# Kernel tuning notes

Measured on AMD Instinct MI355X. Metric: run time of the kernel, lower is better.

## Reference

```python
import jax, jax.numpy as jnp
import numpy as np

B, S, D, H = 2, 2048, 1024, 16
DK = D // H

def setup_inputs() -> dict:
    key = jax.random.key(0)
    ks = jax.random.split(key, 5)
    std = 1.0 / np.sqrt(D)
    return {
        "x": jax.random.normal(ks[0], (B, S, D), dtype=jnp.float32),
        "wq": jax.random.normal(ks[1], (D, D), dtype=jnp.float32) * std,
        "wk": jax.random.normal(ks[2], (D, D), dtype=jnp.float32) * std,
        "wv": jax.random.normal(ks[3], (D, D), dtype=jnp.float32) * std,
        "wo": jax.random.normal(ks[4], (D, D), dtype=jnp.float32) * std,
    }

def reference(x, wq, wk, wv, wo):
    b, s, d = x.shape
    # torch Linear(bias=False): x @ W.T
    q = (x @ wq.T).reshape(b, s, H, DK).transpose(0, 2, 1, 3)  # [b,h,s,dk]
    k = (x @ wk.T).reshape(b, s, H, DK).transpose(0, 2, 1, 3)
    v = (x @ wv.T).reshape(b, s, H, DK).transpose(0, 2, 1, 3)
    scale = jnp.sqrt(jnp.asarray(DK, dtype=x.dtype))
    scores = jnp.einsum('bhqd,bhkd->bhqk', q, k) / scale  # [b,h,s,s]
    # causal mask (masking=True): lower-triangular kept, rest -inf
    causal = jnp.tril(jnp.ones((s, s), dtype=bool))
    scores = jnp.where(causal[None, None], scores, -jnp.inf)
    attn = jax.nn.softmax(scores, axis=-1)
    out = jnp.einsum('bhqk,bhkd->bhqd', attn, v)  # [b,h,s,dk]
    out = out.transpose(0, 2, 1, 3).reshape(b, s, d)
    return out @ wo.T
```

## Files before the change

### kernel.cpp

```cpp
#include <hip/hip_runtime.h>

#define LB __launch_bounds__(256)

typedef __bf16 bf16x8 __attribute__((ext_vector_type(8)));
typedef float f32x4 __attribute__((ext_vector_type(4)));
typedef float f32x16 __attribute__((ext_vector_type(16)));
typedef unsigned int u32;

constexpr int B = 2, S = 2048, D = 1024, H = 16, DK = 64;
constexpr int M = B * S;
constexpr int K = D;

__device__ __forceinline__ unsigned short f2bf(float f) {
    union { float f; unsigned u; } v; v.f = f;
    unsigned r = v.u + 0x7fffu + ((v.u >> 16) & 1u);
    return (unsigned short)(r >> 16);
}

__device__ __forceinline__ u32 pk2bf(float lo, float hi) {
    union { __bf16 h[2]; u32 w; } u;
    u.h[0] = (__bf16)lo; u.h[1] = (__bf16)hi;
    return u.w;
}

__device__ __forceinline__ void gld_lds16(const unsigned short* g, unsigned short* l) {
    __builtin_amdgcn_global_load_lds(
        (const __attribute__((address_space(1))) unsigned int*)g,
        (__attribute__((address_space(3))) unsigned int*)l, 16, 0, 0);
}

__global__ LB void cvt_all(const float* __restrict__ x,  const float* __restrict__ wq,
                           const float* __restrict__ wk, const float* __restrict__ wv,
                           const float* __restrict__ wo, unsigned short* __restrict__ dst) {
    const size_t NX = (size_t)M * D;
    const size_t NW = (size_t)D * D;
    size_t i = ((size_t)blockIdx.x * 256 + threadIdx.x) * 4;
    if (i >= NX + 4 * NW) return;
    const float* src; size_t off;
    if      (i < NX)          { src = x;  off = i; }
    else if (i < NX + NW)     { src = wq; off = i - NX; }
    else if (i < NX + 2 * NW) { src = wk; off = i - NX - NW; }
    else if (i < NX + 3 * NW) { src = wv; off = i - NX - 2 * NW; }
    else                      { src = wo; off = i - NX - 3 * NW; }
    float4 f = *reinterpret_cast<const float4*>(src + off);
    ushort4 o;
    o.x = f2bf(f.x); o.y = f2bf(f.y); o.z = f2bf(f.z); o.w = f2bf(f.w);
    *reinterpret_cast<ushort4*>(dst + i) = o;
}

__global__ LB void gemm_qkv(const unsigned short* __restrict__ A,
                            const unsigned short* __restrict__ wqb,
                            const unsigned short* __restrict__ wkb,
                            const unsigned short* __restrict__ wvb,
                            unsigned short* __restrict__ qo,
                            unsigned short* __restrict__ ko,
                            unsigned short* __restrict__ vo) {
    __shared__ __align__(16) unsigned short lA[128 * 32];
    __shared__ __align__(16) unsigned short lB[128 * 32];
    const int z = blockIdx.y;
    const unsigned short* W = (z == 0) ? wqb : ((z == 1) ? wkb : wvb);
    int m0 = (blockIdx.x >> 3) * 128;
    int n0 = (blockIdx.x & 7) * 128;
    int t = threadIdx.x;
    int w = t >> 6, lane = t & 63;
    int r = lane & 15, g = lane >> 4;
    int wr = w >> 1, wc = w & 1;
    int rowT = t >> 2, colOff = (t & 3) * 8;

    f32x4 acc[4][4];
#pragma unroll
    for (int mi = 0; mi < 4; ++mi)
#pragma unroll
        for (int ni = 0; ni < 4; ++ni) acc[mi][ni] = f32x4{0.f, 0.f, 0.f, 0.f};

    for (int k0 = 0; k0 < K; k0 += 32) {
        gld_lds16(A + (size_t)(m0 + rowT) * K + k0 + colOff,      lA + (w * 64) * 8);
        gld_lds16(A + (size_t)(m0 + 64 + rowT) * K + k0 + colOff, lA + (256 + w * 64) * 8);
        gld_lds16(W + (size_t)(n0 + rowT) * K + k0 + colOff,      lB + (w * 64) * 8);
        gld_lds16(W + (size_t)(n0 + 64 + rowT) * K + k0 + colOff, lB + (256 + w * 64) * 8);
        __syncthreads();
        bf16x8 af[4], bfr[4];
#pragma unroll
        for (int mi = 0; mi < 4; ++mi)
            af[mi] = *reinterpret_cast<const bf16x8*>(&lA[(wr * 64 + mi * 16 + r) * 32 + g * 8]);
#pragma unroll
        for (int ni = 0; ni < 4; ++ni)
            bfr[ni] = *reinterpret_cast<const bf16x8*>(&lB[(wc * 64 + ni * 16 + r) * 32 + g * 8]);
#pragma unroll
        for (int mi = 0; mi < 4; ++mi)
#pragma unroll
            for (int ni = 0; ni < 4; ++ni)
                acc[mi][ni] = __builtin_amdgcn_mfma_f32_16x16x32_bf16(af[mi], bfr[ni], acc[mi][ni], 0, 0, 0);
        __syncthreads();
    }

    const float QSCALE = 0.125f * 1.44269504088896341f;
    float scale = (z == 0) ? QSCALE : 1.0f;
    unsigned short* dst = (z == 0) ? qo : ((z == 1) ? ko : vo);
#pragma unroll
    for (int mi = 0; mi < 4; ++mi)
#pragma unroll
        for (int ni = 0; ni < 4; ++ni)
#pragma unroll
            for (int j = 0; j < 4; ++j) {
                int row = m0 + wr * 64 + mi * 16 + g * 4 + j;
                int col = n0 + wc * 64 + ni * 16 + r;
                int b = row >> 11, s = row & (S - 1);
                int h = col >> 6, dk = col & 63;
                size_t bh = (size_t)(b * H + h);
                unsigned short val = f2bf(acc[mi][ni][j] * scale);
                if (z == 0) {
                    dst[(bh * S + s) * DK + dk] = val;
                } else if (z == 1) {
                    int kt32 = s >> 5, q5k = s & 31;
                    int dsi = dk >> 4, hlk = (dk >> 3) & 1, e = dk & 7;
                    dst[(((bh * 64 + kt32) * 4 + dsi) * 64 + (hlk * 32 + q5k)) * 8 + e] = val;
                } else {
                    int ktile = s >> 6, ks2 = (s >> 4) & 3, hlv = (s >> 3) & 1, e = s & 7;
                    int rh = dk >> 5, q5r = dk & 31;
                    dst[(((bh * 32 + ktile) * 8 + rh * 4 + ks2) * 64 + (hlv * 32 + q5r)) * 8 + e] = val;
                }
            }
}

__global__ LB void out_gemm(const unsigned short* __restrict__ A,
                            const unsigned short* __restrict__ W,
                            float* __restrict__ out) {
    __shared__ __align__(16) unsigned short lA[128 * 32];
    __shared__ __align__(16) unsigned short lB[128 * 32];
    int m0 = (blockIdx.x >> 3) * 128;
    int n0 = (blockIdx.x & 7) * 128;
    int t = threadIdx.x;
    int w = t >> 6, lane = t & 63;
    int r = lane & 15, g = lane >> 4;
    int wr = w >> 1, wc = w & 1;
    int rowT = t >> 2, colOff = (t & 3) * 8;

    f32x4 acc[4][4];
#pragma unroll
    for (int mi = 0; mi < 4; ++mi)
#pragma unroll
        for (int ni = 0; ni < 4; ++ni) acc[mi][ni] = f32x4{0.f, 0.f, 0.f, 0.f};

    for (int k0 = 0; k0 < K; k0 += 32) {
        gld_lds16(A + (size_t)(m0 + rowT) * K + k0 + colOff,      lA + (w * 64) * 8);
        gld_lds16(A + (size_t)(m0 + 64 + rowT) * K + k0 + colOff, lA + (256 + w * 64) * 8);
        gld_lds16(W + (size_t)(n0 + rowT) * K + k0 + colOff,      lB + (w * 64) * 8);
        gld_lds16(W + (size_t)(n0 + 64 + rowT) * K + k0 + colOff, lB + (256 + w * 64) * 8);
        __syncthreads();
        bf16x8 af[4], bfr[4];
#pragma unroll
        for (int mi = 0; mi < 4; ++mi)
            af[mi] = *reinterpret_cast<const bf16x8*>(&lA[(wr * 64 + mi * 16 + r) * 32 + g * 8]);
#pragma unroll
        for (int ni = 0; ni < 4; ++ni)
            bfr[ni] = *reinterpret_cast<const bf16x8*>(&lB[(wc * 64 + ni * 16 + r) * 32 + g * 8]);
#pragma unroll
        for (int mi = 0; mi < 4; ++mi)
#pragma unroll
            for (int ni = 0; ni < 4; ++ni)
                acc[mi][ni] = __builtin_amdgcn_mfma_f32_16x16x32_bf16(af[mi], bfr[ni], acc[mi][ni], 0, 0, 0);
        __syncthreads();
    }

#pragma unroll
    for (int mi = 0; mi < 4; ++mi)
#pragma unroll
        for (int ni = 0; ni < 4; ++ni)
#pragma unroll
            for (int j = 0; j < 4; ++j) {
                int row = m0 + wr * 64 + mi * 16 + g * 4 + j;
                int col = n0 + wc * 64 + ni * 16 + r;
                out[(size_t)row * D + col] = acc[mi][ni][j];
            }
}

__global__ __launch_bounds__(64) void flash_attn(
        const unsigned short* __restrict__ q,
        const unsigned short* __restrict__ kmat,
        const unsigned short* __restrict__ vt,
        unsigned short* __restrict__ ao) {
    int bid = blockIdx.x;
    int kk = bid >> 8, cc = bid & 255;
    int r9 = (kk << 8) | ((kk & 1) ? (255 - cc) : cc);
    int qt = 63 - (r9 >> 5);
    int bh = r9 & 31;
    int b = bh >> 4, hd = bh & 15;
    int q0 = qt << 5;
    int nt = (qt + 2) >> 1;

    int l = threadIdx.x;
    int q5 = l & 31, hl = l >> 5;
    int qglob = q0 + q5;

    const unsigned short* qp = q    + (size_t)bh * S * DK;
    const unsigned short* kf = kmat + (size_t)bh * S * DK;
    const unsigned short* vf = vt   + (size_t)bh * S * DK;

    bf16x8 ones;
#pragma unroll
    for (int i = 0; i < 8; ++i) ones[i] = (__bf16)1.0f;

    const f32x16 z16 = {0,0,0,0,0,0,0,0,0,0,0,0,0,0,0,0};

    bf16x8 qf[4];
#pragma unroll
    for (int dsi = 0; dsi < 4; ++dsi)
        qf[dsi] = *reinterpret_cast<const bf16x8*>(qp + (size_t)qglob * DK + dsi * 16 + hl * 8);

    f32x16 acc0 = z16, acc1 = z16, accl = z16;

    auto loadK = [&](bf16x8 (&kr)[8], int kb) {
        const unsigned short* base = kf + (size_t)(kb >> 5) * 4 * 512 + l * 8;
#pragma unroll
        for (int dsi = 0; dsi < 4; ++dsi) {
            kr[dsi]     = *reinterpret_cast<const bf16x8*>(base + dsi * 512);
            kr[4 + dsi] = *reinterpret_cast<const bf16x8*>(base + (4 + dsi) * 512);
        }
    };
    auto loadV = [&](bf16x8 (&vr)[8], int kb) {
        const unsigned short* base = vf + (size_t)(kb >> 6) * 8 * 512 + l * 8;
#pragma unroll
        for (int i2 = 0; i2 < 8; ++i2)
            vr[i2] = *reinterpret_cast<const bf16x8*>(base + i2 * 512);
    };
    auto compute = [&](bf16x8 (&kr)[8], bf16x8 (&vr)[8], int kb) {
        f32x16 st0 = z16, st1 = z16;
#pragma unroll
        for (int dsi = 0; dsi < 4; ++dsi) {
            st0 = __builtin_amdgcn_mfma_f32_32x32x16_bf16(kr[dsi],     qf[dsi], st0, 0, 0, 0);
            st1 = __builtin_amdgcn_mfma_f32_32x32x16_bf16(kr[4 + dsi], qf[dsi], st1, 0, 0, 0);
        }
        if (kb + 31 > q0) {
#pragma unroll
            for (int r = 0; r < 16; ++r) {
                int kv = kb + (r & 3) + 8 * (r >> 2) + 4 * hl;
                st0[r] = (kv <= qglob) ? st0[r] : -1e30f;
            }
        }
        if (kb + 63 > q0) {
#pragma unroll
            for (int r = 0; r < 16; ++r) {
                int kv = kb + 32 + (r & 3) + 8 * (r >> 2) + 4 * hl;
                st1[r] = (kv <= qglob) ? st1[r] : -1e30f;
            }
        }
#pragma unroll
        for (int r = 0; r < 16; ++r) { st0[r] = exp2f(st0[r]); st1[r] = exp2f(st1[r]); }
        u32 pk[2][8];
#pragma unroll
        for (int rg = 0; rg < 4; ++rg) {
            pk[0][2*rg]   = pk2bf(st0[4*rg],   st0[4*rg+1]);
            pk[0][2*rg+1] = pk2bf(st0[4*rg+2], st0[4*rg+3]);
            pk[1][2*rg]   = pk2bf(st1[4*rg],   st1[4*rg+1]);
            pk[1][2*rg+1] = pk2bf(st1[4*rg+2], st1[4*rg+3]);
        }
        union PF { bf16x8 vv; u32 w[4]; } pf[4];
#pragma unroll
        for (int ti2 = 0; ti2 < 2; ++ti2)
#pragma unroll
            for (int s = 0; s < 2; ++s) {
                u32 s0 = hl ? pk[ti2][4*s]   : pk[ti2][4*s+2];
                u32 s1 = hl ? pk[ti2][4*s+1] : pk[ti2][4*s+3];
                u32 r0 = (u32)__shfl_xor((int)s0, 32);
                u32 r1 = (u32)__shfl_xor((int)s1, 32);
                PF f;
                f.w[0] = hl ? r0 : pk[ti2][4*s];
                f.w[1] = hl ? r1 : pk[ti2][4*s+1];
                f.w[2] = hl ? pk[ti2][4*s+2] : r0;
                f.w[3] = hl ? pk[ti2][4*s+3] : r1;
                pf[ti2*2+s] = f;
            }
#pragma unroll
        for (int ks = 0; ks < 4; ++ks) {
            acc0 = __builtin_amdgcn_mfma_f32_32x32x16_bf16(vr[ks],     pf[ks].vv, acc0, 0, 0, 0);
            acc1 = __builtin_amdgcn_mfma_f32_32x32x16_bf16(vr[4 + ks], pf[ks].vv, acc1, 0, 0, 0);
            accl = __builtin_amdgcn_mfma_f32_32x32x16_bf16(ones,       pf[ks].vv, accl, 0, 0, 0);
        }
    };

    bf16x8 ka[8], kb2[8], va[8], vb2[8];
    loadK(ka, 0);
    loadV(va, 0);
    int it = 0;
    while (true) {
        if (it + 1 < nt) { loadK(kb2, (it + 1) << 6); loadV(vb2, (it + 1) << 6); }
        compute(ka, va, it << 6);
        ++it; if (it >= nt) break;
        if (it + 1 < nt) { loadK(ka, (it + 1) << 6); loadV(va, (it + 1) << 6); }
        compute(kb2, vb2, it << 6);
        ++it; if (it >= nt) break;
    }

    float inv = 1.0f / accl[0];
    size_t obase = ((size_t)(b * S + qglob)) * D + hd * DK;
#pragma unroll
    for (int rg = 0; rg < 4; ++rg) {
        uint2 wd;
        wd.x = pk2bf(acc0[4*rg]   * inv, acc0[4*rg+1] * inv);
        wd.y = pk2bf(acc0[4*rg+2] * inv, acc0[4*rg+3] * inv);
        *reinterpret_cast<uint2*>(ao + obase + rg * 8 + hl * 4) = wd;
        uint2 we;
        we.x = pk2bf(acc1[4*rg]   * inv, acc1[4*rg+1] * inv);
        we.y = pk2bf(acc1[4*rg+2] * inv, acc1[4*rg+3] * inv);
        *reinterpret_cast<uint2*>(ao + obase + 32 + rg * 8 + hl * 4) = we;
    }
}

extern "C" void kernel_launch(void* const* d_in, const int* in_sizes, int n_in,
                              void* d_out, int out_size, void* d_ws, size_t ws_size,
                              hipStream_t stream) {
    const float* x  = (const float*)d_in[0];
    const float* wq = (const float*)d_in[1];
    const float* wk = (const float*)d_in[2];
    const float* wv = (const float*)d_in[3];
    const float* wo = (const float*)d_in[4];
    char* ws = (char*)d_ws;
    unsigned short* xb  = (unsigned short*)(ws);
    unsigned short* wqb = (unsigned short*)(ws + (size_t)(8  << 20));
    unsigned short* wkb = (unsigned short*)(ws + (size_t)(10 << 20));
    unsigned short* wvb = (unsigned short*)(ws + (size_t)(12 << 20));
    unsigned short* wob = (unsigned short*)(ws + (size_t)(14 << 20));
    unsigned short* qb  = (unsigned short*)(ws + (size_t)(16 << 20));
    unsigned short* kb  = (unsigned short*)(ws + (size_t)(24 << 20));
    unsigned short* vtb = (unsigned short*)(ws + (size_t)(32 << 20));
    unsigned short* aob = (unsigned short*)(ws + (size_t)(40 << 20));

    cvt_all<<<8192, 256, 0, stream>>>(x, wq, wk, wv, wo, xb);

    gemm_qkv<<<dim3(256, 3), 256, 0, stream>>>(xb, wqb, wkb, wvb, qb, kb, vtb);
    flash_attn<<<2048, 64, 0, stream>>>(qb, kb, vtb, aob);
    out_gemm<<<256, 256, 0, stream>>>(aob, wob, (float*)d_out);
}
```

Before: 124.8 us.

## Split attention KV loop across two waves per block with LDS merge

The flash attention block grows from one wave to two. Each wave handles alternating 64-key tiles of the causal range, and the partial numerators and denominators are merged through shared memory before wave 0 normalizes and writes the output. The aim is to shorten the serial per-block KV loop and raise the number of waves per CU. The snake-order block remapping is also dropped in favour of a plain linear mapping. The cost is an LDS merge plus a barrier, and the load balance between the two waves is uneven when the tile count is odd.

New measurement: 129.8 us. 4.0% more time.

```diff
diff --git a/kernel.cpp b/kernel.cpp
--- a/kernel.cpp
+++ b/kernel.cpp
@@ -175,21 +175,22 @@
             }
 }
 
-__global__ __launch_bounds__(64) void flash_attn(
+__global__ __launch_bounds__(128) void flash_attn(
         const unsigned short* __restrict__ q,
         const unsigned short* __restrict__ kmat,
         const unsigned short* __restrict__ vt,
         unsigned short* __restrict__ ao) {
+    __shared__ float mrg[64][33];
     int bid = blockIdx.x;
-    int kk = bid >> 8, cc = bid & 255;
-    int r9 = (kk << 8) | ((kk & 1) ? (255 - cc) : cc);
-    int qt = 63 - (r9 >> 5);
-    int bh = r9 & 31;
+    int qt = 63 - (bid >> 5);
+    int bh = bid & 31;
     int b = bh >> 4, hd = bh & 15;
     int q0 = qt << 5;
     int nt = (qt + 2) >> 1;
 
-    int l = threadIdx.x;
+    int tid = threadIdx.x;
+    int w = tid >> 6;
+    int l = tid & 63;
     int q5 = l & 31, hl = l >> 5;
     int qglob = q0 + q5;
 
@@ -280,30 +281,44 @@
     };
 
     bf16x8 ka[8], kb2[8], va[8], vb2[8];
-    loadK(ka, 0);
-    loadV(va, 0);
-    int it = 0;
-    while (true) {
-        if (it + 1 < nt) { loadK(kb2, (it + 1) << 6); loadV(vb2, (it + 1) << 6); }
-        compute(ka, va, it << 6);
-        ++it; if (it >= nt) break;
-        if (it + 1 < nt) { loadK(ka, (it + 1) << 6); loadV(va, (it + 1) << 6); }
-        compute(kb2, vb2, it << 6);
-        ++it; if (it >= nt) break;
-    }
-
-    float inv = 1.0f / accl[0];
-    size_t obase = ((size_t)(b * S + qglob)) * D + hd * DK;
-#pragma unroll
-    for (int rg = 0; rg < 4; ++rg) {
-        uint2 wd;
-        wd.x = pk2bf(acc0[4*rg]   * inv, acc0[4*rg+1] * inv);
-        wd.y = pk2bf(acc0[4*rg+2] * inv, acc0[4*rg+3] * inv);
-        *reinterpret_cast<uint2*>(ao + obase + rg * 8 + hl * 4) = wd;
-        uint2 we;
-        we.x = pk2bf(acc1[4*rg]   * inv, acc1[4*rg+1] * inv);
-        we.y = pk2bf(acc1[4*rg+2] * inv, acc1[4*rg+3] * inv);
-        *reinterpret_cast<uint2*>(ao + obase + 32 + rg * 8 + hl * 4) = we;
+    int it = w;
+    if (it < nt) {
+        loadK(ka, it << 6);
+        loadV(va, it << 6);
+        while (true) {
+            if (it + 2 < nt) { loadK(kb2, (it + 2) << 6); loadV(vb2, (it + 2) << 6); }
+            compute(ka, va, it << 6);
+            it += 2; if (it >= nt) break;
+            if (it + 2 < nt) { loadK(ka, (it + 2) << 6); loadV(va, (it + 2) << 6); }
+            compute(kb2, vb2, it << 6);
+            it += 2; if (it >= nt) break;
+        }
+    }
+
+    if (w == 1) {
+#pragma unroll
+        for (int r = 0; r < 16; ++r) mrg[l][r] = acc0[r];
+#pragma unroll
+        for (int r = 0; r < 16; ++r) mrg[l][16 + r] = acc1[r];
+        mrg[l][32] = accl[0];
+    }
+    __syncthreads();
+    if (w == 0) {
+#pragma unroll
+        for (int r = 0; r < 16; ++r) { acc0[r] += mrg[l][r]; acc1[r] += mrg[l][16 + r]; }
+        float inv = 1.0f / (accl[0] + mrg[l][32]);
+        size_t obase = ((size_t)(b * S + qglob)) * D + hd * DK;
+#pragma unroll
+        for (int rg = 0; rg < 4; ++rg) {
+            uint2 wd;
+            wd.x = pk2bf(acc0[4*rg]   * inv, acc0[4*rg+1] * inv);
+            wd.y = pk2bf(acc0[4*rg+2] * inv, acc0[4*rg+3] * inv);
+            *reinterpret_cast<uint2*>(ao + obase + rg * 8 + hl * 4) = wd;
+            uint2 we;
+            we.x = pk2bf(acc1[4*rg]   * inv, acc1[4*rg+1] * inv);
+            we.y = pk2bf(acc1[4*rg+2] * inv, acc1[4*rg+3] * inv);
+            *reinterpret_cast<uint2*>(ao + obase + 32 + rg * 8 + hl * 4) = we;
+        }
     }
 }
 
@@ -329,6 +344,6 @@
     cvt_all<<<8192, 256, 0, stream>>>(x, wq, wk, wv, wo, xb);
 
     gemm_qkv<<<dim3(256, 3), 256, 0, stream>>>(xb, wqb, wkb, wvb, qb, kb, vtb);
-    flash_attn<<<2048, 64, 0, stream>>>(qb, kb, vtb, aob);
+    flash_attn<<<2048, 128, 0, stream>>>(qb, kb, vtb, aob);
     out_gemm<<<256, 256, 0, stream>>>(aob, wob, (float*)d_out);
 }
```

## Stage K/V epilogue through LDS for coalesced stores and raise MFMA wave priority

Applied to the files above, without the earlier changes.

The QKV GEMM epilogue for K and V now writes the accumulator tile into a padded shared-memory buffer, one half at a time, and then emits 16-byte vectorized stores in the swizzled fragment layout the attention kernel expects. Before, each thread wrote scattered 2-byte values. The attention kernel also wraps its MFMA sections in s_setprio so waves issuing matrix ops get scheduling priority over waves doing softmax work. In exchange, the GEMM kernel needs about 18KB of extra LDS, which can lower occupancy, and adds barriers around the staging.

New measurement: 156.8 us. +25.6%, slower.

```diff
diff --git a/kernel.cpp b/kernel.cpp
--- a/kernel.cpp
+++ b/kernel.cpp
@@ -57,6 +57,7 @@
                             unsigned short* __restrict__ vo) {
     __shared__ __align__(16) unsigned short lA[128 * 32];
     __shared__ __align__(16) unsigned short lB[128 * 32];
+    __shared__ __align__(16) unsigned short lT[9216];
     const int z = blockIdx.y;
     const unsigned short* W = (z == 0) ? wqb : ((z == 1) ? wkb : wvb);
     int m0 = (blockIdx.x >> 3) * 128;
@@ -94,33 +95,79 @@
         __syncthreads();
     }
 
-    const float QSCALE = 0.125f * 1.44269504088896341f;
-    float scale = (z == 0) ? QSCALE : 1.0f;
-    unsigned short* dst = (z == 0) ? qo : ((z == 1) ? ko : vo);
-#pragma unroll
-    for (int mi = 0; mi < 4; ++mi)
-#pragma unroll
-        for (int ni = 0; ni < 4; ++ni)
-#pragma unroll
-            for (int j = 0; j < 4; ++j) {
-                int row = m0 + wr * 64 + mi * 16 + g * 4 + j;
-                int col = n0 + wc * 64 + ni * 16 + r;
-                int b = row >> 11, s = row & (S - 1);
-                int h = col >> 6, dk = col & 63;
-                size_t bh = (size_t)(b * H + h);
-                unsigned short val = f2bf(acc[mi][ni][j] * scale);
-                if (z == 0) {
-                    dst[(bh * S + s) * DK + dk] = val;
-                } else if (z == 1) {
-                    int kt32 = s >> 5, q5k = s & 31;
-                    int dsi = dk >> 4, hlk = (dk >> 3) & 1, e = dk & 7;
-                    dst[(((bh * 64 + kt32) * 4 + dsi) * 64 + (hlk * 32 + q5k)) * 8 + e] = val;
-                } else {
-                    int ktile = s >> 6, ks2 = (s >> 4) & 3, hlv = (s >> 3) & 1, e = s & 7;
-                    int rh = dk >> 5, q5r = dk & 31;
-                    dst[(((bh * 32 + ktile) * 8 + rh * 4 + ks2) * 64 + (hlv * 32 + q5r)) * 8 + e] = val;
+    if (z == 0) {
+        const float QSCALE = 0.125f * 1.44269504088896341f;
+#pragma unroll
+        for (int mi = 0; mi < 4; ++mi)
+#pragma unroll
+            for (int ni = 0; ni < 4; ++ni)
+#pragma unroll
+                for (int j = 0; j < 4; ++j) {
+                    int row = m0 + wr * 64 + mi * 16 + g * 4 + j;
+                    int col = n0 + wc * 64 + ni * 16 + r;
+                    int b = row >> 11, s = row & (S - 1);
+                    int h = col >> 6, dk = col & 63;
+                    qo[(((size_t)(b * H + h)) * S + s) * DK + dk] = f2bf(acc[mi][ni][j] * QSCALE);
                 }
-            }
+    } else if (z == 1) {
+#pragma unroll 1
+        for (int Hh = 0; Hh < 2; ++Hh) {
+            __syncthreads();
+            if (wr == Hh) {
+#pragma unroll
+                for (int mi = 0; mi < 4; ++mi)
+#pragma unroll
+                    for (int ni = 0; ni < 4; ++ni)
+#pragma unroll
+                        for (int j = 0; j < 4; ++j)
+                            lT[(mi * 16 + g * 4 + j) * 136 + wc * 64 + ni * 16 + r] =
+                                f2bf(acc[mi][ni][j]);
+            }
+            __syncthreads();
+            int base_s = (m0 & (S - 1)) + Hh * 64;
+            int bbig = (m0 + Hh * 64) >> 11;
+#pragma unroll
+            for (int c = 0; c < 4; ++c) {
+                int chunk = w * 4 + c;
+                int kt32l = chunk >> 3, headl = (chunk >> 2) & 1, dsi = chunk & 3;
+                int s_local = kt32l * 32 + (lane & 31);
+                int colb = headl * 64 + dsi * 16 + (lane >> 5) * 8;
+                int kt32g = (base_s >> 5) + kt32l;
+                size_t bh2 = (size_t)(bbig * H + (n0 >> 6) + headl);
+                uint4 v4 = *reinterpret_cast<const uint4*>(&lT[s_local * 136 + colb]);
+                *reinterpret_cast<uint4*>(ko + (((bh2 * 64 + kt32g) * 4 + dsi) * 64 + lane) * 8) = v4;
+            }
+        }
+    } else {
+#pragma unroll 1
+        for (int Hh = 0; Hh < 2; ++Hh) {
+            __syncthreads();
+            if (wr == Hh) {
+#pragma unroll
+                for (int mi = 0; mi < 4; ++mi)
+#pragma unroll
+                    for (int ni = 0; ni < 4; ++ni)
+#pragma unroll
+                        for (int j = 0; j < 4; ++j)
+                            lT[(wc * 64 + ni * 16 + r) * 72 + mi * 16 + g * 4 + j] =
+                                f2bf(acc[mi][ni][j]);
+            }
+            __syncthreads();
+            int base_s = (m0 & (S - 1)) + Hh * 64;
+            int ktile = base_s >> 6;
+            int bbig = (m0 + Hh * 64) >> 11;
+#pragma unroll
+            for (int c = 0; c < 4; ++c) {
+                int chunk = w * 4 + c;
+                int headl = chunk >> 3, rh = (chunk >> 2) & 1, ks2 = chunk & 3;
+                int dk_local = headl * 64 + rh * 32 + (lane & 31);
+                int s_off = ks2 * 16 + (lane >> 5) * 8;
+                size_t bh2 = (size_t)(bbig * H + (n0 >> 6) + headl);
+                uint4 v4 = *reinterpret_cast<const uint4*>(&lT[dk_local * 72 + s_off]);
+                *reinterpret_cast<uint4*>(vo + (((bh2 * 32 + ktile) * 8 + rh * 4 + ks2) * 64 + lane) * 8) = v4;
+            }
+        }
+    }
 }
 
 __global__ LB void out_gemm(const unsigned short* __restrict__ A,
@@ -226,11 +273,13 @@
     };
     auto compute = [&](bf16x8 (&kr)[8], bf16x8 (&vr)[8], int kb) {
         f32x16 st0 = z16, st1 = z16;
+        __builtin_amdgcn_s_setprio(1);
 #pragma unroll
         for (int dsi = 0; dsi < 4; ++dsi) {
             st0 = __builtin_amdgcn_mfma_f32_32x32x16_bf16(kr[dsi],     qf[dsi], st0, 0, 0, 0);
             st1 = __builtin_amdgcn_mfma_f32_32x32x16_bf16(kr[4 + dsi], qf[dsi], st1, 0, 0, 0);
         }
+        __builtin_amdgcn_s_setprio(0);
         if (kb + 31 > q0) {
 #pragma unroll
             for (int r = 0; r < 16; ++r) {
@@ -271,12 +320,14 @@
                 f.w[3] = hl ? pk[ti2][4*s+3] : r1;
                 pf[ti2*2+s] = f;
             }
+        __builtin_amdgcn_s_setprio(1);
 #pragma unroll
         for (int ks = 0; ks < 4; ++ks) {
             acc0 = __builtin_amdgcn_mfma_f32_32x32x16_bf16(vr[ks],     pf[ks].vv, acc0, 0, 0, 0);
             acc1 = __builtin_amdgcn_mfma_f32_32x32x16_bf16(vr[4 + ks], pf[ks].vv, acc1, 0, 0, 0);
             accl = __builtin_amdgcn_mfma_f32_32x32x16_bf16(ones,       pf[ks].vv, accl, 0, 0, 0);
         }
+        __builtin_amdgcn_s_setprio(0);
     };
 
     bf16x8 ka[8], kb2[8], va[8], vb2[8];
```
